# Kernel tuning notes

Hardware: AMD Instinct MI355X
Metric: run time of the kernel (lower is better)

Reference implementation:

```python
import jax, jax.numpy as jnp
import numpy as np

B, S, D, H = 512, 200, 512, 8
FF = 1024          # dim_feedforward == hidden_dim
EMB, HID, FIN = 128, 1024, 64
V = 100000
QK_SCALE, ATTN_CLIP, FFN_CLIP, QKV_CLIP = 0.05, 3.0, 2.0, 1.0
PAD = 0


def _ln(x, g, b, eps=1e-6):
    m = jnp.mean(x, -1, keepdims=True)
    v = jnp.mean((x - m) ** 2, -1, keepdims=True)
    return (x - m) / jnp.sqrt(v + eps) * g + b


def setup_inputs() -> dict:
    key = jax.random.key(0)
    ks = jax.random.split(key, 32)
    n = lambda i, shape, s=0.02: (s * jax.random.normal(ks[i], shape)).astype(jnp.float32)
    emb_table = n(0, (V, D)).at[PAD].set(0.0)  # padding row zeroed
    inp = {
        'item_seq': jax.random.randint(ks[20], (B, S), 0, V),
        'user_avg_ctr': jax.random.uniform(ks[21], (B,)),
        'user_total_interactions': jax.random.uniform(ks[22], (B,)),
        'age_price': jax.random.randint(ks[23], (B,), 0, 100),
        'gender_cate': jax.random.randint(ks[24], (B,), 0, 10),
        'cms_group_id': jax.random.randint(ks[25], (B,), 0, 13),
        'emb_table': emb_table,
        'in_proj_w': n(1, (3 * D, D)),
        'out_proj_w': n(2, (D, D)),
        'out_proj_b': jnp.zeros((D,), jnp.float32),
        'ln1_g': jnp.ones((D,), jnp.float32), 'ln1_b': jnp.zeros((D,), jnp.float32),
        'ln2_g': jnp.ones((D,), jnp.float32), 'ln2_b': jnp.zeros((D,), jnp.float32),
        'lin1_w': n(3, (FF, D)), 'lin1_b': jnp.zeros((FF,), jnp.float32),
        'lin2_w': n(4, (D, FF)), 'lin2_b': jnp.zeros((D,), jnp.float32),
        'age_tab': n(5, (100, EMB)), 'gender_tab': n(6, (10, EMB)), 'cms_tab': n(7, (13, EMB)),
        'ctr_w': n(8, (EMB, 1)), 'ctr_b': jnp.zeros((EMB,), jnp.float32),
        'ti_w': n(9, (EMB, 1)), 'ti_b': jnp.zeros((EMB,), jnp.float32),
        'mlp1_w': n(10, (HID, D + 5 * EMB)), 'mlp1_b': jnp.zeros((HID,), jnp.float32),
        'mlp2_w': n(11, (FIN, HID)), 'mlp2_b': jnp.zeros((FIN,), jnp.float32),
    }
    return inp


def reference(item_seq, user_avg_ctr, user_total_interactions, age_price, gender_cate,
              cms_group_id, emb_table, in_proj_w, out_proj_w, out_proj_b,
              ln1_g, ln1_b, ln2_g, ln2_b, lin1_w, lin1_b, lin2_w, lin2_b,
              age_tab, gender_tab, cms_tab, ctr_w, ctr_b, ti_w, ti_b,
              mlp1_w, mlp1_b, mlp2_w, mlp2_b):
    dk = D // H
    pad = item_seq == PAD  # [B,S] key padding mask
    x = jnp.clip(emb_table[item_seq] * 0.5, -1.0, 1.0)  # [B,S,D]

    # ---- custom self-attention block (no in_proj bias, heavy clamping) ----
    qw, kw, vw = in_proj_w[:D], in_proj_w[D:2 * D], in_proj_w[2 * D:]
    q = jnp.clip(x @ qw.T, -QKV_CLIP, QKV_CLIP)
    k = jnp.clip(x @ kw.T, -QKV_CLIP, QKV_CLIP)
    v = jnp.clip(x @ vw.T, -QKV_CLIP, QKV_CLIP)
    q = q.reshape(B, S, H, dk).transpose(0, 2, 1, 3)
    k = k.reshape(B, S, H, dk).transpose(0, 2, 1, 3)
    v = v.reshape(B, S, H, dk).transpose(0, 2, 1, 3)
    scores = jnp.einsum('bhqd,bhkd->bhqk', q, k) / (np.float32(np.sqrt(dk)) * QK_SCALE)
    scores = jnp.clip(scores, -ATTN_CLIP, ATTN_CLIP)
    scores = jnp.where(pad[:, None, None, :], -1e9, scores)
    w = jax.nn.softmax(scores, axis=-1)  # dropout is identity in eval
    x2 = jnp.einsum('bhqk,bhkd->bhqd', w, v).transpose(0, 2, 1, 3).reshape(B, S, D)
    x2 = jnp.clip(x2 @ out_proj_w.T + out_proj_b, -ATTN_CLIP, ATTN_CLIP)
    sa = _ln(x + x2, ln1_g, ln1_b)          # norm1 inside overridden _sa_block
    x = _ln(x + sa, ln1_g, ln1_b)           # base post-norm wraps norm1 again

    # ---- FFN block with clamps ----
    h = jax.nn.relu(jnp.clip(x @ lin1_w.T + lin1_b, -FFN_CLIP, FFN_CLIP))
    f2 = jnp.clip(h @ lin2_w.T + lin2_b, -FFN_CLIP, FFN_CLIP)
    ff = _ln(x + f2, ln2_g, ln2_b)          # norm2 inside overridden _ff_block
    x = _ln(x + ff, ln2_g, ln2_b)           # base wraps norm2 again

    seq_out = jnp.clip(x, -5.0, 5.0)
    m = (~pad).astype(seq_out.dtype)[:, :, None]
    seq_rep = jnp.clip((seq_out * m).sum(1) / (m.sum(1) + 1e-8), -5.0, 5.0)  # [B,D]

    ape = age_tab[age_price]
    ge = gender_tab[gender_cate]
    ce = cms_tab[cms_group_id]
    ctr = user_avg_ctr[:, None] @ ctr_w.T + ctr_b
    ti = user_total_interactions[:, None] @ ti_w.T + ti_b
    u = jnp.concatenate([seq_rep, ctr, ti, ape, ge, ce], axis=-1)  # [B, D+5*EMB]
    return jax.nn.relu(u @ mlp1_w.T + mlp1_b) @ mlp2_w.T + mlp2_b  # [B, FIN]
```

## Files before the change

### kernel.cpp

```cpp
#include <hip/hip_runtime.h>
#include <hip/hip_bf16.h>
#include <stdint.h>

typedef __attribute__((ext_vector_type(8))) short short8;
typedef __attribute__((ext_vector_type(4))) float f32x4;
typedef unsigned short u16;

#define MFMA16(a,b,c) __builtin_amdgcn_mfma_f32_16x16x32_bf16((a),(b),(c),0,0,0)

__device__ __forceinline__ u16 f2bf(float f) {
  unsigned int u = __float_as_uint(f);
  return (u16)((u + 0x7FFFu + ((u >> 16) & 1u)) >> 16);
}
__device__ __forceinline__ float bf2f(u16 h) {
  return __uint_as_float(((unsigned int)h) << 16);
}
__device__ __forceinline__ float clampf(float v, float lo, float hi) {
  return fminf(fmaxf(v, lo), hi);
}
__device__ __forceinline__ void gl2lds16(const u16* g, u16* l) {
  __builtin_amdgcn_global_load_lds(
      (const __attribute__((address_space(1))) unsigned int*)g,
      (__attribute__((address_space(3))) unsigned int*)(uintptr_t)l,
      16, 0, 0);
}

__global__ __launch_bounds__(256) void cvt_bf16_kernel(
    const float* __restrict__ src, u16* __restrict__ dst, int n) {
  for (int i = blockIdx.x*256 + threadIdx.x; i < n; i += gridDim.x*256)
    dst[i] = f2bf(src[i]);
}

__global__ __launch_bounds__(256) void embed_kernel(
    const int* __restrict__ iseq, const float* __restrict__ emb,
    u16* __restrict__ xb) {
  int gid = blockIdx.x*256 + threadIdx.x;
  int m = gid >> 7;
  int c = (gid & 127) * 4;
  int item = iseq[m];
  float4 e = *(const float4*)&emb[(size_t)item*512 + c];
  ushort4 hb;
  hb.x = f2bf(clampf(e.x*0.5f, -1.f, 1.f));
  hb.y = f2bf(clampf(e.y*0.5f, -1.f, 1.f));
  hb.z = f2bf(clampf(e.z*0.5f, -1.f, 1.f));
  hb.w = f2bf(clampf(e.w*0.5f, -1.f, 1.f));
  *(ushort4*)&xb[(size_t)m*512 + c] = hb;
}

__global__ __launch_bounds__(256) void cnt_kernel(
    const int* __restrict__ item_seq, float* __restrict__ cnt) {
  __shared__ int sred[4];
  int b = blockIdx.x, tid = threadIdx.x;
  int lane = tid & 63, wv = tid >> 6;
  int c = 0;
  if (tid < 200) c = (item_seq[b*200 + tid] != 0) ? 1 : 0;
  #pragma unroll
  for (int m = 1; m <= 32; m <<= 1) c += __shfl_xor(c, m);
  if (lane == 0) sred[wv] = c;
  __syncthreads();
  if (tid == 0) cnt[b] = (float)(sred[0]+sred[1]+sred[2]+sred[3]);
}

#define BAR() asm volatile("s_barrier" ::: "memory")
#define LGKM0() do { asm volatile("s_waitcnt lgkmcnt(0)" ::: "memory"); \
                     __builtin_amdgcn_sched_barrier(0); } while (0)
#define VMW(N) asm volatile("s_waitcnt vmcnt(" #N ")" ::: "memory")

__device__ __forceinline__ void stage_half(const char* gsrc0, size_t rstride,
                                           u16* lhalf, int wv, int lane) {
  #pragma unroll
  for (int j = 0; j < 2; ++j) {
    const int o   = j*8192 + wv*1024 + lane*16;
    const int row = o >> 7;
    const int cb  = (o & 127) ^ ((row & 7) << 4);
    gl2lds16((const u16*)(gsrc0 + (size_t)row*rstride + cb),
             (u16*)((char*)lhalf + j*8192 + wv*1024));
  }
}

__device__ __forceinline__ short8 ldsfrag(const u16* slot, int row, int kb) {
  return *(const short8*)((const char*)slot + row*128 + (kb ^ ((row & 7) << 4)));
}

template <int MODE>
__global__ __launch_bounds__(512, 2)
void gemm_bt(const u16* __restrict__ A, const u16* __restrict__ Bw,
             const float* __restrict__ bias, int K, int Nt, int swz,
             u16* __restrict__ outB, u16* __restrict__ QKV, long long projStride) {
  __shared__ __align__(16) u16 SH[34816];
  u16* const As0 = SH;
  u16* const As1 = SH + 16384;
  const int tid  = threadIdx.x;
  const int lane = tid & 63;
  const int wv   = tid >> 6;
  const int wm   = wv >> 2;
  const int wn   = wv & 3;
  const int id   = blockIdx.x;
  int mt, nt2;
  if (swz) { mt = (id / (8*Nt))*8 + (id & 7); nt2 = (id >> 3) % Nt; }
  else     { mt = id / Nt;                    nt2 = id % Nt; }
  const int m0 = mt * 256;
  const int n0 = nt2 * 256;
  const int KT = K >> 6;

  const char* Abase = (const char*)(A  + (size_t)m0*K);
  const char* Bbase = (const char*)(Bw + (size_t)n0*K);
  const size_t rs = (size_t)K * 2;

  const int r16 = lane & 15;
  const int q4  = lane >> 4;
  const size_t browB = (size_t)(wn*64 + r16)*rs + q4*16;

  const f32x4 fz = {0.f, 0.f, 0.f, 0.f};
  f32x4 acc[8][4];
  #pragma unroll
  for (int i = 0; i < 8; ++i)
    #pragma unroll
    for (int j = 0; j < 4; ++j) acc[i][j] = fz;

  short8 af[4][2];
  short8 bfA[4][2], bfB[4][2];

  #pragma unroll
  for (int nf = 0; nf < 4; ++nf)
    #pragma unroll
    for (int ks = 0; ks < 2; ++ks)
      bfA[nf][ks] = *(const short8*)(Bbase + browB + (size_t)nf*16*rs + ks*64);
  stage_half(Abase,              rs, As0,            wv, lane);
  stage_half(Abase + 128*rs,     rs, As0 + 128*64,   wv, lane);
  stage_half(Abase + 128,        rs, As1,            wv, lane);
  VMW(2);
  BAR();

  auto kstep = [&](int t, u16* Acur, u16* Aoth,
                   short8 (&bfC)[4][2], short8 (&bfN)[4][2]) {
    const bool l1 = (t + 1 < KT);
    const bool l2 = (t + 2 < KT);
    const char* Bg1 = Bbase + (size_t)(t+1)*128;
    const char* Ag1 = Abase + (size_t)(t+1)*128;
    const char* Ag2 = Abase + (size_t)(t+2)*128;
    if (l1) {
      #pragma unroll
      for (int nf = 0; nf < 4; ++nf)
        #pragma unroll
        for (int ks = 0; ks < 2; ++ks)
          bfN[nf][ks] = *(const short8*)(Bg1 + browB + (size_t)nf*16*rs + ks*64);
    }
    #pragma unroll
    for (int i = 0; i < 4; ++i)
      #pragma unroll
      for (int ks = 0; ks < 2; ++ks)
        af[i][ks] = ldsfrag(Acur, wm*128 + i*16 + r16, ks*64 + q4*16);
    if (l1) stage_half(Ag1 + 128*rs, rs, Aoth + 128*64, wv, lane);
    BAR(); LGKM0();
    __builtin_amdgcn_s_setprio(1);
    #pragma unroll
    for (int i = 0; i < 4; ++i)
      #pragma unroll
      for (int nf = 0; nf < 4; ++nf)
        #pragma unroll
        for (int ks = 0; ks < 2; ++ks)
          acc[i][nf] = MFMA16(af[i][ks], bfC[nf][ks], acc[i][nf]);
    __builtin_amdgcn_s_setprio(0);
    if (l1) { VMW(12); } else { VMW(0); }
    BAR();
    #pragma unroll
    for (int i = 0; i < 4; ++i)
      #pragma unroll
      for (int ks = 0; ks < 2; ++ks)
        af[i][ks] = ldsfrag(Acur, wm*128 + 64 + i*16 + r16, ks*64 + q4*16);
    if (l2) stage_half(Ag2, rs, Acur, wv, lane);
    BAR(); LGKM0();
    __builtin_amdgcn_s_setprio(1);
    #pragma unroll
    for (int i = 0; i < 4; ++i)
      #pragma unroll
      for (int nf = 0; nf < 4; ++nf)
        #pragma unroll
        for (int ks = 0; ks < 2; ++ks)
          acc[4+i][nf] = MFMA16(af[i][ks], bfC[nf][ks], acc[4+i][nf]);
    __builtin_amdgcn_s_setprio(0);
    if (l2) { VMW(12); } else if (l1) { VMW(10); }
    BAR();
  };

  const int NI = KT >> 1;
  for (int it = 0; it < NI; ++it) {
    kstep(it*2,     As0, As1, bfA, bfB);
    kstep(it*2 + 1, As1, As0, bfB, bfA);
  }

  {
    u16* const L = SH;
    const int LROW = 272;
    #pragma unroll
    for (int h = 0; h < 2; ++h) {
      if (h == 1) __syncthreads();
      if (wm == h) {
        #pragma unroll
        for (int nf = 0; nf < 4; ++nf) {
          const int col_l = wn*64 + nf*16 + r16;
          const float bvs = (MODE == 0) ? 0.f : bias[n0 + col_l];
          #pragma unroll
          for (int mi = 0; mi < 8; ++mi) {
            const int row_l = mi*16 + q4*4;
            #pragma unroll
            for (int r = 0; r < 4; ++r) {
              float v = acc[mi][nf][r];
              if (MODE == 0)      v = clampf(v, -1.f, 1.f);
              else if (MODE == 1) v = clampf(v + bvs, -3.f, 3.f);
              else if (MODE == 2) v = fmaxf(clampf(v + bvs, -2.f, 2.f), 0.f);
              else                v = clampf(v + bvs, -2.f, 2.f);
              L[(row_l + r)*LROW + col_l] = f2bf(v);
            }
          }
        }
      }
      __syncthreads();
      #pragma unroll
      for (int k = 0; k < 8; ++k) {
        const int ch   = wv*512 + k*64 + lane;
        const int row  = ch >> 5;
        const int colu = (ch & 31) * 8;
        short8 d = *(const short8*)&L[row*LROW + colu];
        const int rowg = m0 + h*128 + row;
        const int cg   = n0 + colu;
        if (MODE == 0) {
          const unsigned proj = (unsigned)cg >> 9;
          const unsigned hh   = ((unsigned)cg >> 6) & 7u;
          const unsigned dk   = (unsigned)cg & 63u;
          const int b = rowg / 200;
          const int s = rowg - b*200;
          *(short8*)&QKV[(size_t)proj*projStride + (size_t)hh*12800
                         + (size_t)b*102400 + (size_t)s*64 + dk] = d;
        } else {
          const int N = (MODE == 2) ? 1024 : 512;
          *(short8*)&outB[(size_t)rowg*N + cg] = d;
        }
      }
    }
  }
}

__global__ __launch_bounds__(512)
void attn_kernel(const u16* __restrict__ Q, const u16* __restrict__ K,
                 const u16* __restrict__ V, const int* __restrict__ iseq,
                 u16* __restrict__ x2b) {
  __shared__ __align__(16) u16 Ks[208*72];
  __shared__ __align__(16) u16 Vs[64*232];
  __shared__ __align__(16) u16 Ps[8][16*40];
  __shared__ float msk[208];

  const int tid = threadIdx.x, lane = tid & 63, wv = tid >> 6;
  const unsigned bid = blockIdx.x;
  const int h = bid & 7;
  const int b = bid >> 3;
  const size_t bh = (size_t)b*8 + h;
  const u16* Kg = K + bh*12800;
  const u16* Vg = V + bh*12800;
  const u16* Qg = Q + bh*12800;

  for (int c = tid; c < 3200; c += 512) {
    int row = c >> 4, q = c & 15;
    *(ushort4*)&Ks[row*72 + q*4] = *(const ushort4*)&Kg[row*64 + q*4];
  }
  {
    const int quad = wv*2 + (lane >> 5);
    const int sl   = lane & 31;
    #pragma unroll
    for (int it = 0; it < 7; ++it) {
      const int s = sl + it*32;
      if (s < 200) {
        ushort4 v4 = *(const ushort4*)&Vg[s*64 + quad*4];
        Vs[(quad*4+0)*232 + s] = v4.x;
        Vs[(quad*4+1)*232 + s] = v4.y;
        Vs[(quad*4+2)*232 + s] = v4.z;
        Vs[(quad*4+3)*232 + s] = v4.w;
      }
    }
  }
  for (int c = tid; c < 2048; c += 512) {
    int dk = c >> 5, s2 = 200 + (c & 31);
    Vs[dk*232 + s2] = 0;
  }
  for (int t = tid; t < 208; t += 512)
    msk[t] = (t < 200 && iseq[b*200 + t] != 0) ? 1.f : 0.f;
  __syncthreads();

  const int colk = lane & 15;
  const int fk8 = (lane >> 4) * 8;
  const int prow = (lane >> 4) * 4;
  const f32x4 fz = {0.f,0.f,0.f,0.f};

  for (int qb = 0; qb < 2; ++qb) {
    const int qrow = qb*128 + wv*16 + (lane & 15);
    const int qsrc = qrow < 200 ? qrow : 199;
    short8 qa0 = *(const short8*)&Qg[(size_t)qsrc*64 + fk8];
    short8 qa1 = *(const short8*)&Qg[(size_t)qsrc*64 + 32 + fk8];
    f32x4 oacc[4];
    #pragma unroll
    for (int nt = 0; nt < 4; ++nt) oacc[nt] = fz;
    float rs[4] = {0.f,0.f,0.f,0.f};

    for (int kt2 = 0; kt2 < 7; ++kt2) {
      #pragma unroll
      for (int half = 0; half < 2; ++half) {
        const int stile = kt2*2 + half;
        if (stile < 13) {
          const int key = stile*16 + colk;
          short8 kb0 = *(const short8*)&Ks[key*72 + fk8];
          short8 kb1 = *(const short8*)&Ks[key*72 + 32 + fk8];
          f32x4 sc = fz;
          __builtin_amdgcn_s_setprio(1);
          sc = MFMA16(qa0, kb0, sc);
          sc = MFMA16(qa1, kb1, sc);
          __builtin_amdgcn_s_setprio(0);
          const float mk = msk[key];
          #pragma unroll
          for (int r = 0; r < 4; ++r) {
            float p = __expf(clampf(sc[r]*2.5f, -3.f, 3.f)) * mk;
            rs[r] += p;
            Ps[wv][(prow + r)*40 + half*16 + colk] = f2bf(p);
          }
        } else {
          #pragma unroll
          for (int r = 0; r < 4; ++r)
            Ps[wv][(prow + r)*40 + half*16 + colk] = 0;
        }
      }
      asm volatile("s_waitcnt lgkmcnt(0)" ::: "memory");
      short8 pa = *(const short8*)&Ps[wv][(lane & 15)*40 + fk8];
      const int kb32 = kt2*32;
      __builtin_amdgcn_s_setprio(1);
      #pragma unroll
      for (int nt = 0; nt < 4; ++nt) {
        short8 vb = *(const short8*)&Vs[(nt*16 + colk)*232 + kb32 + fk8];
        oacc[nt] = MFMA16(pa, vb, oacc[nt]);
      }
      __builtin_amdgcn_s_setprio(0);
      asm volatile("s_waitcnt lgkmcnt(0)" ::: "memory");
    }

    #pragma unroll
    for (int m = 1; m <= 8; m <<= 1)
      #pragma unroll
      for (int r = 0; r < 4; ++r) rs[r] += __shfl_xor(rs[r], m);

    const int srow = qb*128 + wv*16 + prow;
    #pragma unroll
    for (int r = 0; r < 4; ++r) {
      const int s = srow + r;
      if (s < 200) {
        const float inv = rs[r] > 0.f ? 1.f/rs[r] : 0.f;
        const size_t base = ((size_t)b*200 + s)*512 + h*64;
        #pragma unroll
        for (int nt = 0; nt < 4; ++nt)
          x2b[base + nt*16 + colk] = f2bf(oacc[nt][r] * inv);
      }
    }
  }
}

__global__ __launch_bounds__(256)
void ln1_kernel(const u16* __restrict__ xb, const u16* __restrict__ x2b,
                const float* __restrict__ g, const float* __restrict__ bb,
                u16* __restrict__ xnb) {
  const int lane = threadIdx.x & 63, wv = threadIdx.x >> 6;
  const size_t t = (size_t)blockIdx.x*4 + wv;
  const int c0 = lane*4, c1 = 256 + lane*4;
  ushort4 xa = *(const ushort4*)&xb[t*512 + c0];
  ushort4 xc = *(const ushort4*)&xb[t*512 + c1];
  ushort4 ha = *(const ushort4*)&x2b[t*512 + c0];
  ushort4 hc = *(const ushort4*)&x2b[t*512 + c1];
  float xv[8] = {bf2f(xa.x),bf2f(xa.y),bf2f(xa.z),bf2f(xa.w),
                 bf2f(xc.x),bf2f(xc.y),bf2f(xc.z),bf2f(xc.w)};
  float tv[8] = {xv[0]+bf2f(ha.x), xv[1]+bf2f(ha.y), xv[2]+bf2f(ha.z), xv[3]+bf2f(ha.w),
                 xv[4]+bf2f(hc.x), xv[5]+bf2f(hc.y), xv[6]+bf2f(hc.z), xv[7]+bf2f(hc.w)};
  float s1 = 0.f, s2 = 0.f;
  #pragma unroll
  for (int i = 0; i < 8; ++i) { s1 += tv[i]; s2 += tv[i]*tv[i]; }
  #pragma unroll
  for (int m = 1; m <= 32; m <<= 1) { s1 += __shfl_xor(s1, m); s2 += __shfl_xor(s2, m); }
  float mean = s1*(1.f/512.f);
  float inv = 1.f/sqrtf(s2*(1.f/512.f) - mean*mean + 1e-6f);
  float4 ga = *(const float4*)(g + c0), gc = *(const float4*)(g + c1);
  float4 ba = *(const float4*)(bb + c0), bc = *(const float4*)(bb + c1);
  float gv[8] = {ga.x,ga.y,ga.z,ga.w, gc.x,gc.y,gc.z,gc.w};
  float bv[8] = {ba.x,ba.y,ba.z,ba.w, bc.x,bc.y,bc.z,bc.w};
  float uv[8]; float s3 = 0.f, s4 = 0.f;
  #pragma unroll
  for (int i = 0; i < 8; ++i) {
    float sa = (tv[i]-mean)*inv*gv[i] + bv[i];
    uv[i] = xv[i] + sa;
    s3 += uv[i]; s4 += uv[i]*uv[i];
  }
  #pragma unroll
  for (int m = 1; m <= 32; m <<= 1) { s3 += __shfl_xor(s3, m); s4 += __shfl_xor(s4, m); }
  float mean2 = s3*(1.f/512.f);
  float inv2 = 1.f/sqrtf(s4*(1.f/512.f) - mean2*mean2 + 1e-6f);
  ushort4 o0, o1;
  o0.x = f2bf((uv[0]-mean2)*inv2*gv[0] + bv[0]);
  o0.y = f2bf((uv[1]-mean2)*inv2*gv[1] + bv[1]);
  o0.z = f2bf((uv[2]-mean2)*inv2*gv[2] + bv[2]);
  o0.w = f2bf((uv[3]-mean2)*inv2*gv[3] + bv[3]);
  o1.x = f2bf((uv[4]-mean2)*inv2*gv[4] + bv[4]);
  o1.y = f2bf((uv[5]-mean2)*inv2*gv[5] + bv[5]);
  o1.z = f2bf((uv[6]-mean2)*inv2*gv[6] + bv[6]);
  o1.w = f2bf((uv[7]-mean2)*inv2*gv[7] + bv[7]);
  *(ushort4*)&xnb[t*512 + c0] = o0;
  *(ushort4*)&xnb[t*512 + c1] = o1;
}

__global__ __launch_bounds__(256)
void ln2_kernel(const u16* __restrict__ xnb, const u16* __restrict__ f2b,
                const float* __restrict__ g, const float* __restrict__ bb,
                const int* __restrict__ iseq, float* __restrict__ seq_acc) {
  const int tid = threadIdx.x, lane = tid & 63, wv = tid >> 6;
  const int q = blockIdx.x, bl = blockIdx.y;
  const int c8 = lane*8;
  float gv[8], bv[8];
  *(float4*)&gv[0] = *(const float4*)(g + c8);
  *(float4*)&gv[4] = *(const float4*)(g + c8 + 4);
  *(float4*)&bv[0] = *(const float4*)(bb + c8);
  *(float4*)&bv[4] = *(const float4*)(bb + c8 + 4);
  float acc[8] = {};
  for (int i = wv; i < 50; i += 4) {
    const int s = q*50 + i;
    const size_t row = (size_t)bl*200 + s;
    short8 xh = *(const short8*)&xnb[row*512 + c8];
    short8 yh = *(const short8*)&f2b[row*512 + c8];
    float xv[8], tv[8];
    #pragma unroll
    for (int j = 0; j < 8; ++j) {
      xv[j] = bf2f((u16)xh[j]);
      tv[j] = xv[j] + bf2f((u16)yh[j]);
    }
    float s1 = 0.f, s2 = 0.f;
    #pragma unroll
    for (int j = 0; j < 8; ++j) { s1 += tv[j]; s2 += tv[j]*tv[j]; }
    #pragma unroll
    for (int m = 1; m <= 32; m <<= 1) { s1 += __shfl_xor(s1,m); s2 += __shfl_xor(s2,m); }
    float mean = s1*(1.f/512.f);
    float inv = 1.f/sqrtf(s2*(1.f/512.f) - mean*mean + 1e-6f);
    float uv[8]; float s3 = 0.f, s4 = 0.f;
    #pragma unroll
    for (int j = 0; j < 8; ++j) {
      uv[j] = xv[j] + (tv[j]-mean)*inv*gv[j] + bv[j];
      s3 += uv[j]; s4 += uv[j]*uv[j];
    }
    #pragma unroll
    for (int m = 1; m <= 32; m <<= 1) { s3 += __shfl_xor(s3,m); s4 += __shfl_xor(s4,m); }
    float mean2 = s3*(1.f/512.f);
    float inv2 = 1.f/sqrtf(s4*(1.f/512.f) - mean2*mean2 + 1e-6f);
    if (iseq[row] != 0) {
      #pragma unroll
      for (int j = 0; j < 8; ++j)
        acc[j] += clampf((uv[j]-mean2)*inv2*gv[j] + bv[j], -5.f, 5.f);
    }
  }
  float* dst = &seq_acc[(((size_t)bl*4 + q)*4 + wv)*512 + c8];
  *(float4*)&dst[0] = *(float4*)&acc[0];
  *(float4*)&dst[4] = *(float4*)&acc[4];
}

__global__ __launch_bounds__(256)
void build_u_kernel(const float* __restrict__ seq_acc, const float* __restrict__ cnt,
                    const float* __restrict__ uac, const float* __restrict__ uti,
                    const int* __restrict__ age, const int* __restrict__ gen,
                    const int* __restrict__ cms,
                    const float* __restrict__ age_tab, const float* __restrict__ gen_tab,
                    const float* __restrict__ cms_tab,
                    const float* __restrict__ ctr_w, const float* __restrict__ ctr_b,
                    const float* __restrict__ ti_w, const float* __restrict__ ti_b,
                    float* __restrict__ u) {
  const int b = blockIdx.x;
  for (int j = threadIdx.x; j < 1152; j += 256) {
    float v;
    if (j < 512) {
      float ssum = 0.f;
      #pragma unroll
      for (int p = 0; p < 16; ++p) ssum += seq_acc[((size_t)b*16 + p)*512 + j];
      v = clampf(ssum / (cnt[b] + 1e-8f), -5.f, 5.f);
    }
    else if (j < 640)  { int e = j-512;  v = uac[b]*ctr_w[e] + ctr_b[e]; }
    else if (j < 768)  { int e = j-640;  v = uti[b]*ti_w[e] + ti_b[e]; }
    else if (j < 896)  { int e = j-768;  v = age_tab[age[b]*128 + e]; }
    else if (j < 1024) { int e = j-896;  v = gen_tab[gen[b]*128 + e]; }
    else               { int e = j-1024; v = cms_tab[cms[b]*128 + e]; }
    u[(size_t)b*1152 + j] = v;
  }
}

__global__ __launch_bounds__(256)
void mlp1_kernel(const float* __restrict__ u, const float* __restrict__ w,
                 const float* __restrict__ bias, float* __restrict__ h1) {
  __shared__ __align__(16) float As[64][36];
  __shared__ __align__(16) float Wt[32][68];
  const int tid = threadIdx.x;
  const int m0 = blockIdx.x*64, n0 = blockIdx.y*64;
  const int tm = tid >> 4, tn = tid & 15;
  float acc[4][4] = {};
  for (int k0 = 0; k0 < 1152; k0 += 32) {
    for (int c = tid; c < 512; c += 256) {
      int row = c >> 3, q = c & 7;
      *(float4*)&As[row][q*4] = *(const float4*)&u[(size_t)(m0+row)*1152 + k0 + q*4];
      float4 wv4 = *(const float4*)&w[(size_t)(n0+row)*1152 + k0 + q*4];
      Wt[q*4+0][row] = wv4.x; Wt[q*4+1][row] = wv4.y;
      Wt[q*4+2][row] = wv4.z; Wt[q*4+3][row] = wv4.w;
    }
    __syncthreads();
    #pragma unroll
    for (int kk = 0; kk < 32; ++kk) {
      float av[4], bw[4];
      #pragma unroll
      for (int i = 0; i < 4; ++i) av[i] = As[tm*4+i][kk];
      #pragma unroll
      for (int j = 0; j < 4; ++j) bw[j] = Wt[kk][tn*4+j];
      #pragma unroll
      for (int i = 0; i < 4; ++i)
        #pragma unroll
        for (int j = 0; j < 4; ++j) acc[i][j] += av[i]*bw[j];
    }
    __syncthreads();
  }
  #pragma unroll
  for (int i = 0; i < 4; ++i)
    #pragma unroll
    for (int j = 0; j < 4; ++j) {
      int n = n0 + tn*4 + j;
      h1[(size_t)(m0 + tm*4 + i)*1024 + n] = fmaxf(acc[i][j] + bias[n], 0.f);
    }
}

__global__ __launch_bounds__(256)
void mlp2_kernel(const float* __restrict__ h1, const float* __restrict__ w,
                 const float* __restrict__ bias, float* __restrict__ out) {
  const int tid = threadIdx.x;
  const int m = blockIdx.x*4 + (tid >> 6);
  const int n = tid & 63;
  const float4* hr = (const float4*)(h1 + (size_t)m*1024);
  const float4* wr = (const float4*)(w + (size_t)n*1024);
  float acc = 0.f;
  for (int k4 = 0; k4 < 256; ++k4) {
    float4 a = hr[k4], bw = wr[k4];
    acc += a.x*bw.x + a.y*bw.y + a.z*bw.z + a.w*bw.w;
  }
  out[(size_t)m*64 + n] = acc + bias[n];
}

extern "C" void kernel_launch(void* const* d_in, const int* in_sizes, int n_in,
                              void* d_out, int out_size, void* d_ws, size_t ws_size,
                              hipStream_t stream) {
  (void)in_sizes; (void)n_in; (void)out_size;
  const int*   item_seq   = (const int*)d_in[0];
  const float* uac        = (const float*)d_in[1];
  const float* uti        = (const float*)d_in[2];
  const int*   age        = (const int*)d_in[3];
  const int*   gen        = (const int*)d_in[4];
  const int*   cms        = (const int*)d_in[5];
  const float* emb        = (const float*)d_in[6];
  const float* in_proj_w  = (const float*)d_in[7];
  const float* out_proj_w = (const float*)d_in[8];
  const float* out_proj_b = (const float*)d_in[9];
  const float* ln1_g = (const float*)d_in[10];
  const float* ln1_b = (const float*)d_in[11];
  const float* ln2_g = (const float*)d_in[12];
  const float* ln2_b = (const float*)d_in[13];
  const float* lin1_w = (const float*)d_in[14];
  const float* lin1_b = (const float*)d_in[15];
  const float* lin2_w = (const float*)d_in[16];
  const float* lin2_b = (const float*)d_in[17];
  const float* age_tab = (const float*)d_in[18];
  const float* gen_tab = (const float*)d_in[19];
  const float* cms_tab = (const float*)d_in[20];
  const float* ctr_w = (const float*)d_in[21];
  const float* ctr_b = (const float*)d_in[22];
  const float* ti_w  = (const float*)d_in[23];
  const float* ti_b  = (const float*)d_in[24];
  const float* mlp1_w = (const float*)d_in[25];
  const float* mlp1_b = (const float*)d_in[26];
  const float* mlp2_w = (const float*)d_in[27];
  const float* mlp2_b = (const float*)d_in[28];

  const long long TAILB = 25430016LL;
  int CB = 32;
  if      ((long long)ws_size >= 512LL*1024000 + TAILB) CB = 512;
  else if ((long long)ws_size >= 128LL*1024000 + TAILB) CB = 128;
  else if ((long long)ws_size >=  64LL*1024000 + TAILB) CB = 64;
  const long long R = (long long)CB * 204800;

  char* ws = (char*)d_ws;
  u16* xb   = (u16*)(ws);
  u16* x2b  = (u16*)(ws + R);
  u16* Qb   = (u16*)(ws + 2*R);
  u16* Kb   = (u16*)(ws + 3*R);
  u16* Vrb  = (u16*)(ws + 4*R);
  u16* x2o  = Qb;
  u16* xnb  = Kb;
  u16* f2b  = Vrb;
  u16* hbuf = (u16*)(ws);
  char* tail = ws + 5*R;
  float* seq_acc = (float*)(tail);
  float* cnt     = (float*)(tail + 16777216);
  float* u       = (float*)(tail + 16779264);
  float* h1      = (float*)(tail + 19138560);
  u16*   wqkv    = (u16*)(tail + 21235712);
  u16*   wout    = (u16*)(tail + 22808576);
  u16*   wl1     = (u16*)(tail + 23332864);
  u16*   wl2     = (u16*)(tail + 24381440);

  cvt_bf16_kernel<<<768, 256, 0, stream>>>(in_proj_w, wqkv, 1536*512);
  cvt_bf16_kernel<<<256, 256, 0, stream>>>(out_proj_w, wout, 512*512);
  cvt_bf16_kernel<<<512, 256, 0, stream>>>(lin1_w, wl1, 1024*512);
  cvt_bf16_kernel<<<512, 256, 0, stream>>>(lin2_w, wl2, 512*1024);
  cnt_kernel<<<512, 256, 0, stream>>>(item_seq, cnt);

  const int nch = 512 / CB;
  const int Mc  = CB * 200;
  const int Mt  = Mc / 256;
  const int swz = (Mt % 8 == 0) ? 1 : 0;
  const long long projStride = (long long)CB * 102400;
  for (int ch = 0; ch < nch; ++ch) {
    const int* iseq = item_seq + (size_t)ch*CB*200;
    embed_kernel<<<Mc/2, 256, 0, stream>>>(iseq, emb, xb);
    gemm_bt<0><<<Mt*6, 512, 0, stream>>>(xb, wqkv, nullptr, 512, 6, swz,
                                         nullptr, Qb, projStride);
    attn_kernel<<<CB*8, 512, 0, stream>>>(Qb, Kb, Vrb, iseq, x2b);
    gemm_bt<1><<<Mt*2, 512, 0, stream>>>(x2b, wout, out_proj_b, 512, 2, swz,
                                         x2o, nullptr, 0);
    ln1_kernel<<<Mc/4, 256, 0, stream>>>(xb, x2o, ln1_g, ln1_b, xnb);
    gemm_bt<2><<<Mt*4, 512, 0, stream>>>(xnb, wl1, lin1_b, 512, 4, swz,
                                         hbuf, nullptr, 0);
    gemm_bt<3><<<Mt*2, 512, 0, stream>>>(hbuf, wl2, lin2_b, 1024, 2, swz,
                                         f2b, nullptr, 0);
    ln2_kernel<<<dim3(4, CB), 256, 0, stream>>>(xnb, f2b, ln2_g, ln2_b, iseq,
                                                seq_acc + (size_t)ch*CB*8192);
  }

  build_u_kernel<<<512, 256, 0, stream>>>(seq_acc, cnt, uac, uti, age, gen, cms,
                                          age_tab, gen_tab, cms_tab,
                                          ctr_w, ctr_b, ti_w, ti_b, u);
  mlp1_kernel<<<dim3(8, 16), 256, 0, stream>>>(u, mlp1_w, mlp1_b, h1);
  mlp2_kernel<<<128, 256, 0, stream>>>(h1, mlp2_w, mlp2_b, (float*)d_out);
}
```

Before: 1.649 ms.

## Stage both A and B tiles in LDS with single-buffered synchronous K loop

Replaces the double-buffered A-in-LDS pipeline, where B fragments were prefetched from global memory into registers, with a simple loop. Each K step loads both A and B tiles into LDS, waits for all loads, computes, then loads the next step. This removes B register prefetching and shrinks LDS use, but drops the overlap of global loads with MFMA compute, so each iteration stalls on memory. The epilogue LDS row pitch also changes from 272 to 256, which may bring back bank conflicts.

```diff
diff --git a/kernel.cpp b/kernel.cpp
--- a/kernel.cpp
+++ b/kernel.cpp
@@ -62,8 +62,6 @@
 }
 
 #define BAR() asm volatile("s_barrier" ::: "memory")
-#define LGKM0() do { asm volatile("s_waitcnt lgkmcnt(0)" ::: "memory"); \
-                     __builtin_amdgcn_sched_barrier(0); } while (0)
 #define VMW(N) asm volatile("s_waitcnt vmcnt(" #N ")" ::: "memory")
 
 __device__ __forceinline__ void stage_half(const char* gsrc0, size_t rstride,
@@ -87,9 +85,9 @@
 void gemm_bt(const u16* __restrict__ A, const u16* __restrict__ Bw,
              const float* __restrict__ bias, int K, int Nt, int swz,
              u16* __restrict__ outB, u16* __restrict__ QKV, long long projStride) {
-  __shared__ __align__(16) u16 SH[34816];
-  u16* const As0 = SH;
-  u16* const As1 = SH + 16384;
+  __shared__ __align__(16) u16 SH[32768];
+  u16* const As = SH;
+  u16* const Bs = SH + 16384;
   const int tid  = threadIdx.x;
   const int lane = tid & 63;
   const int wv   = tid >> 6;
@@ -109,7 +107,6 @@
 
   const int r16 = lane & 15;
   const int q4  = lane >> 4;
-  const size_t browB = (size_t)(wn*64 + r16)*rs + q4*16;
 
   const f32x4 fz = {0.f, 0.f, 0.f, 0.f};
   f32x4 acc[8][4];
@@ -118,81 +115,59 @@
     #pragma unroll
     for (int j = 0; j < 4; ++j) acc[i][j] = fz;
 
-  short8 af[4][2];
-  short8 bfA[4][2], bfB[4][2];
-
-  #pragma unroll
-  for (int nf = 0; nf < 4; ++nf)
-    #pragma unroll
-    for (int ks = 0; ks < 2; ++ks)
-      bfA[nf][ks] = *(const short8*)(Bbase + browB + (size_t)nf*16*rs + ks*64);
-  stage_half(Abase,              rs, As0,            wv, lane);
-  stage_half(Abase + 128*rs,     rs, As0 + 128*64,   wv, lane);
-  stage_half(Abase + 128,        rs, As1,            wv, lane);
-  VMW(2);
+  short8 af[2][4][2];
+  short8 bf[4][2];
+
+  stage_half(Abase,            rs, As,           wv, lane);
+  stage_half(Abase + 128*rs,   rs, As + 128*64,  wv, lane);
+  stage_half(Bbase,            rs, Bs,           wv, lane);
+  stage_half(Bbase + 128*rs,   rs, Bs + 128*64,  wv, lane);
+  VMW(0);
   BAR();
 
-  auto kstep = [&](int t, u16* Acur, u16* Aoth,
-                   short8 (&bfC)[4][2], short8 (&bfN)[4][2]) {
-    const bool l1 = (t + 1 < KT);
-    const bool l2 = (t + 2 < KT);
-    const char* Bg1 = Bbase + (size_t)(t+1)*128;
-    const char* Ag1 = Abase + (size_t)(t+1)*128;
-    const char* Ag2 = Abase + (size_t)(t+2)*128;
-    if (l1) {
-      #pragma unroll
-      for (int nf = 0; nf < 4; ++nf)
+  for (int t = 0; t < KT; ++t) {
+    #pragma unroll
+    for (int h = 0; h < 2; ++h)
+      #pragma unroll
+      for (int i = 0; i < 4; ++i)
         #pragma unroll
         for (int ks = 0; ks < 2; ++ks)
-          bfN[nf][ks] = *(const short8*)(Bg1 + browB + (size_t)nf*16*rs + ks*64);
-    }
-    #pragma unroll
-    for (int i = 0; i < 4; ++i)
+          af[h][i][ks] = ldsfrag(As, wm*128 + h*64 + i*16 + r16, ks*64 + q4*16);
+    #pragma unroll
+    for (int nf = 0; nf < 4; ++nf)
       #pragma unroll
       for (int ks = 0; ks < 2; ++ks)
-        af[i][ks] = ldsfrag(Acur, wm*128 + i*16 + r16, ks*64 + q4*16);
-    if (l1) stage_half(Ag1 + 128*rs, rs, Aoth + 128*64, wv, lane);
-    BAR(); LGKM0();
+        bf[nf][ks] = ldsfrag(Bs, wn*64 + nf*16 + r16, ks*64 + q4*16);
+
     __builtin_amdgcn_s_setprio(1);
     #pragma unroll
-    for (int i = 0; i < 4; ++i)
-      #pragma unroll
-      for (int nf = 0; nf < 4; ++nf)
+    for (int h = 0; h < 2; ++h)
+      #pragma unroll
+      for (int i = 0; i < 4; ++i)
         #pragma unroll
-        for (int ks = 0; ks < 2; ++ks)
-          acc[i][nf] = MFMA16(af[i][ks], bfC[nf][ks], acc[i][nf]);
+        for (int nf = 0; nf < 4; ++nf)
+          #pragma unroll
+          for (int ks = 0; ks < 2; ++ks)
+            acc[h*4 + i][nf] = MFMA16(af[h][i][ks], bf[nf][ks], acc[h*4 + i][nf]);
     __builtin_amdgcn_s_setprio(0);
-    if (l1) { VMW(12); } else { VMW(0); }
-    BAR();
-    #pragma unroll
-    for (int i = 0; i < 4; ++i)
-      #pragma unroll
-      for (int ks = 0; ks < 2; ++ks)
-        af[i][ks] = ldsfrag(Acur, wm*128 + 64 + i*16 + r16, ks*64 + q4*16);
-    if (l2) stage_half(Ag2, rs, Acur, wv, lane);
-    BAR(); LGKM0();
-    __builtin_amdgcn_s_setprio(1);
-    #pragma unroll
-    for (int i = 0; i < 4; ++i)
-      #pragma unroll
-      for (int nf = 0; nf < 4; ++nf)
-        #pragma unroll
-        for (int ks = 0; ks < 2; ++ks)
-          acc[4+i][nf] = MFMA16(af[i][ks], bfC[nf][ks], acc[4+i][nf]);
-    __builtin_amdgcn_s_setprio(0);
-    if (l2) { VMW(12); } else if (l1) { VMW(10); }
-    BAR();
-  };
-
-  const int NI = KT >> 1;
-  for (int it = 0; it < NI; ++it) {
-    kstep(it*2,     As0, As1, bfA, bfB);
-    kstep(it*2 + 1, As1, As0, bfB, bfA);
-  }
-
+
+    if (t + 1 < KT) {
+      BAR();
+      const char* Ag = Abase + (size_t)(t+1)*128;
+      const char* Bg = Bbase + (size_t)(t+1)*128;
+      stage_half(Ag,            rs, As,           wv, lane);
+      stage_half(Ag + 128*rs,   rs, As + 128*64,  wv, lane);
+      stage_half(Bg,            rs, Bs,           wv, lane);
+      stage_half(Bg + 128*rs,   rs, Bs + 128*64,  wv, lane);
+      VMW(0);
+      BAR();
+    }
+  }
+
+  __syncthreads();
   {
     u16* const L = SH;
-    const int LROW = 272;
+    const int LROW = 256;
     #pragma unroll
     for (int h = 0; h < 2; ++h) {
       if (h == 1) __syncthreads();
```

Result: faster. 1.539 ms (-6.7%).
